# Kernel optimization log

Hardware: AMD Instinct MI355X
Metric: run time of the kernel (lower is better)

Reference implementation:

```python
import jax, jax.numpy as jnp
import numpy as np

D_IN, H, V = 512, 1024, 32000
S, B, T = 64, 128, 48
MARGIN = 0.1


def setup_inputs() -> dict:
    key = jax.random.key(0)
    ks = jax.random.split(key, 16)
    sc = 0.05
    f = lambda k, shp: jax.random.normal(k, shp, jnp.float32) * sc
    emb_W = f(ks[0], (V, D_IN)).at[0].set(0.0)  # padding_idx=0 row is zero
    return dict(
        ctx=jax.random.normal(ks[1], (S, B, H), jnp.float32),
        ctx_mask=jnp.ones((S, B), jnp.float32),
        y=jax.random.randint(ks[2], (T, B), 0, V),
        emb_W=emb_W,
        W_init=f(ks[3], (H, H)), b_init=jnp.zeros((H,), jnp.float32),
        W_ih0=f(ks[4], (3 * H, D_IN)), W_hh0=f(ks[5], (3 * H, H)),
        b_ih0=jnp.zeros((3 * H,), jnp.float32), b_hh0=jnp.zeros((3 * H,), jnp.float32),
        W_c2c=f(ks[6], (H, H)), W_h2c=f(ks[7], (H, H)), v_att=f(ks[8], (H,)),
        W_ih1=f(ks[9], (3 * H, H)), W_hh1=f(ks[10], (3 * H, H)),
        b_ih1=jnp.zeros((3 * H,), jnp.float32), b_hh1=jnp.zeros((3 * H,), jnp.float32),
        W_h2o=f(ks[11], (D_IN, H)), b_h2o=jnp.zeros((D_IN,), jnp.float32),
        W_out=f(ks[12], (V, D_IN)),
    )


def _gru(x, h, Wih, Whh, bih, bhh):
    # torch.nn.GRUCell math
    gi = x @ Wih.T + bih
    gh = h @ Whh.T + bhh
    ir, iz, inn = jnp.split(gi, 3, axis=-1)
    hr, hz, hn = jnp.split(gh, 3, axis=-1)
    r = jax.nn.sigmoid(ir + hr)
    z = jax.nn.sigmoid(iz + hz)
    n = jnp.tanh(inn + r * hn)
    return (1.0 - z) * n + z * h


def reference(ctx, ctx_mask, y, emb_W, W_init, b_init, W_ih0, W_hh0, b_ih0, b_hh0,
              W_c2c, W_h2c, v_att, W_ih1, W_hh1, b_ih1, b_hh1, W_h2o, b_h2o, W_out):
    # dec_init='mean_ctx': tanh(FF(masked mean over source))
    mean_ctx = ctx.sum(0) / ctx_mask.sum(0)[:, None]            # (B,H)
    h = jnp.tanh(mean_ctx @ W_init.T + b_init)                  # h0 (B,H)

    ctx_p = jnp.einsum('sbc,dc->sbd', ctx, W_c2c)               # ctx2ctx, hoisted out of loop
    neg = jnp.where(ctx_mask > 0, 0.0, -1e9)                    # (S,B) additive mask
    W_out_n = W_out / jnp.linalg.norm(W_out, axis=-1, keepdims=True)

    emb_in = emb_W[y[:-1]]                                      # (T-1,B,D_IN)
    targets = y[1:]                                             # (T-1,B)

    def step(h, inp):
        e, tgt = inp
        h1 = _gru(e, h, W_ih0, W_hh0, b_ih0, b_hh0)             # dec0
        # MLP attention: v^T tanh(ctx2ctx(ctx) + hid2ctx(h1))
        scores = jnp.tanh(ctx_p + (h1 @ W_h2c.T)[None]) @ v_att + neg   # (S,B)
        alpha = jax.nn.softmax(scores, axis=0)
        z_t = jnp.einsum('sb,sbc->bc', alpha, ctx)              # context (B,H)
        h2 = _gru(z_t, h1, W_ih1, W_hh1, b_ih1, b_hh1)          # dec1
        logit = jnp.tanh(h2 @ W_h2o.T + b_h2o)                  # hid2out
        logit = logit / jnp.linalg.norm(logit, axis=-1, keepdims=True)
        log_p = logit @ W_out_n.T                               # (B,V) cosine sims
        # max-margin loss, contrastive_type='max', ignore pad (tgt==0)
        s_true = jnp.take_along_axis(log_p, tgt[:, None], axis=1)
        viol = jnp.maximum(MARGIN - s_true + log_p, 0.0)
        viol = viol * (1.0 - jax.nn.one_hot(tgt, V, dtype=log_p.dtype))
        l = jnp.sum(jnp.where(tgt != 0, viol.max(-1), 0.0))
        return h2, l

    _, losses = jax.lax.scan(step, h, (emb_in, targets))
    return losses.sum()
```

## Files before the change

kernel.cpp:

```cpp
#include <hip/hip_runtime.h>
#include <math.h>

#define H    1024
#define H3   3072
#define DIN  512
#define VSZ  32000
#define SS   64
#define BB   128
#define TP   47
#define NROWS (TP*BB)
#define VCHUNKS 250
#define FMARGIN 0.1f
#define NBLK 256
#define HS   65536

typedef unsigned short u16;
typedef unsigned int u32;
typedef __bf16 bf16_t;
typedef bf16_t bf16x8 __attribute__((ext_vector_type(8)));
typedef float f32x4 __attribute__((ext_vector_type(4)));
typedef u16 u16x4 __attribute__((ext_vector_type(4)));
typedef u16 u16x8 __attribute__((ext_vector_type(8)));

#define MFMA __builtin_amdgcn_mfma_f32_16x16x32_bf16

__device__ inline u16 f2bf(float f){
    unsigned b = __float_as_uint(f);
    return (u16)((b + 0x7FFFu + ((b >> 16) & 1u)) >> 16);
}
__device__ inline float bf2f(u16 u){ return __uint_as_float(((unsigned)u) << 16); }
__device__ inline float sigm(float x){ return 1.f/(1.f + expf(-x)); }

__device__ inline void stoval(float* p, float v){ *p = v; }
__device__ inline void stoval(u16* p, float v){ *p = f2bf(v); }

__device__ inline void cstore(u32* p, u32 v){ __hip_atomic_store(p, v, __ATOMIC_RELAXED, __HIP_MEMORY_SCOPE_AGENT); }
__device__ inline void cstoref(float* p, float v){ __hip_atomic_store(p, v, __ATOMIC_RELAXED, __HIP_MEMORY_SCOPE_AGENT); }
__device__ inline float cloadf(const float* p){ return __hip_atomic_load(p, __ATOMIC_RELAXED, __HIP_MEMORY_SCOPE_AGENT); }

__device__ inline void gbar(u32* bar, u32* mygen, int tid){
    __syncthreads();
    if (tid == 0){
        u32 tgt = ++(*mygen);
        __builtin_amdgcn_s_waitcnt(0);
        u32 old = __hip_atomic_fetch_add(&bar[0], 1u, __ATOMIC_RELAXED, __HIP_MEMORY_SCOPE_AGENT);
        if (old == NBLK - 1u){
            __hip_atomic_store(&bar[0], 0u, __ATOMIC_RELAXED, __HIP_MEMORY_SCOPE_AGENT);
            __hip_atomic_store(&bar[1], tgt, __ATOMIC_RELAXED, __HIP_MEMORY_SCOPE_AGENT);
        } else {
            while (__hip_atomic_load(&bar[1], __ATOMIC_RELAXED, __HIP_MEMORY_SCOPE_AGENT) < tgt)
                __builtin_amdgcn_s_sleep(2);
        }
    }
    __syncthreads();
    asm volatile("" ::: "memory");
}


__global__ __launch_bounds__(128) void k_mask_sum(const float* __restrict__ mask, float* __restrict__ msum){
    int b = threadIdx.x;
    if (b < BB){ float s = 0.f; for (int i = 0; i < SS; i++) s += mask[i*BB + b]; msum[b] = s; }
}

__global__ __launch_bounds__(256) void k_mean_ctx(const float* __restrict__ ctx, const float* __restrict__ msum,
                                                  float* __restrict__ mean){
    int idx = blockIdx.x*256 + threadIdx.x;
    if (idx < BB*H){
        float s = 0.f;
        for (int i = 0; i < SS; i++) s += ctx[(size_t)i*BB*H + idx];
        mean[idx] = s / msum[idx / H];
    }
}

__global__ __launch_bounds__(256) void k_f32bf(const float* __restrict__ in, u16* __restrict__ out, int n4){
    int i = blockIdx.x*256 + threadIdx.x;
    if (i >= n4) return;
    float4 v = ((const float4*)in)[i];
    u16x4 o = { f2bf(v.x), f2bf(v.y), f2bf(v.z), f2bf(v.w) };
    ((u16x4*)out)[i] = o;
}

__global__ __launch_bounds__(256) void k_pack_h0(const float* __restrict__ h0, u32* __restrict__ hsHI,
                                                 u32* __restrict__ hsLO, float* __restrict__ hsF){
    int i = blockIdx.x*256 + threadIdx.x;
    float v0 = h0[i*2], v1 = h0[i*2 + 1];
    u16 a = f2bf(v0), b = f2bf(v1);
    hsHI[i] = (u32)a | ((u32)b << 16);
    hsLO[i] = (u32)f2bf(v0 - bf2f(a)) | ((u32)f2bf(v1 - bf2f(b)) << 16);
    hsF[i*2] = v0; hsF[i*2 + 1] = v1;
}

__global__ __launch_bounds__(256) void k_f2bf_frag(const float* __restrict__ in, u16* __restrict__ out,
                                                   int RK8, int K8){
    int t = blockIdx.x*256 + threadIdx.x;
    if (t >= RK8) return;
    int r = t / K8, k8 = t - r*K8;
    const float* p = in + (size_t)r*K8*8 + k8*8;
    float4 a = *(const float4*)p;
    float4 b = *(const float4*)(p + 4);
    size_t dst = ((size_t)(r >> 4)*(K8 >> 2) + (k8 >> 2))*512 + (size_t)((r & 15) + (k8 & 3)*16)*8;
    u16x8 o;
    o[0]=f2bf(a.x); o[1]=f2bf(a.y); o[2]=f2bf(a.z); o[3]=f2bf(a.w);
    o[4]=f2bf(b.x); o[5]=f2bf(b.y); o[6]=f2bf(b.z); o[7]=f2bf(b.w);
    *(u16x8*)(out + dst) = o;
}

__global__ __launch_bounds__(256) void k_rownorm_frag(const float* __restrict__ in, u16* __restrict__ out,
                                                      int nrows){
    int w = threadIdx.x >> 6, lane = threadIdx.x & 63;
    int row = blockIdx.x*4 + w;
    if (row >= nrows) return;
    const float* r = in + (size_t)row*512 + lane*8;
    float4 a = *(const float4*)r;
    float4 b = *(const float4*)(r + 4);
    float s = a.x*a.x + a.y*a.y + a.z*a.z + a.w*a.w
            + b.x*b.x + b.y*b.y + b.z*b.z + b.w*b.w;
    #pragma unroll
    for (int off = 32; off; off >>= 1) s += __shfl_xor(s, off);
    float inv = rsqrtf(s);
    size_t dst = ((size_t)(row >> 4)*16 + (lane >> 2))*512 + (size_t)((row & 15) + (lane & 3)*16)*8;
    u16x8 o;
    o[0]=f2bf(a.x*inv); o[1]=f2bf(a.y*inv); o[2]=f2bf(a.z*inv); o[3]=f2bf(a.w*inv);
    o[4]=f2bf(b.x*inv); o[5]=f2bf(b.y*inv); o[6]=f2bf(b.z*inv); o[7]=f2bf(b.w*inv);
    *(u16x8*)(out + dst) = o;
}

__global__ __launch_bounds__(256) void k_emb_frag(const float* __restrict__ emb, const int* __restrict__ y,
                                                  u16* __restrict__ out){
    int w = threadIdx.x >> 6, lane = threadIdx.x & 63;
    int row = blockIdx.x*4 + w;
    int src = y[row];
    const float* r = emb + (size_t)src*512 + lane*8;
    float4 a = *(const float4*)r;
    float4 b = *(const float4*)(r + 4);
    size_t dst = ((size_t)(row >> 4)*16 + (lane >> 2))*512 + (size_t)((row & 15) + (lane & 3)*16)*8;
    u16x8 o;
    o[0]=f2bf(a.x); o[1]=f2bf(a.y); o[2]=f2bf(a.z); o[3]=f2bf(a.w);
    o[4]=f2bf(b.x); o[5]=f2bf(b.y); o[6]=f2bf(b.z); o[7]=f2bf(b.w);
    *(u16x8*)(out + dst) = o;
}

template<int ACT>
__global__ __launch_bounds__(256) void k_gemm_nt(const float* __restrict__ A, const float* __restrict__ W,
                                                 const float* __restrict__ bias, float* __restrict__ C,
                                                 int M, int N, int K){
    __shared__ float As[16][68];
    __shared__ float Ws[16][68];
    int tid = threadIdx.x;
    int bm = blockIdx.y*64, bn = blockIdx.x*64;
    int lr = tid >> 2;
    int lk = (tid & 3) * 4;
    int tr = (tid >> 4) * 4;
    int tc = (tid & 15) * 4;
    float acc[4][4] = {};
    const float* Abase = A + (size_t)(bm + lr)*K;
    const float* Wbase = W + (size_t)(bn + lr)*K;
    for (int k0 = 0; k0 < K; k0 += 16){
        float4 av = *(const float4*)(Abase + k0 + lk);
        float4 wv = *(const float4*)(Wbase + k0 + lk);
        __syncthreads();
        As[lk+0][lr]=av.x; As[lk+1][lr]=av.y; As[lk+2][lr]=av.z; As[lk+3][lr]=av.w;
        Ws[lk+0][lr]=wv.x; Ws[lk+1][lr]=wv.y; Ws[lk+2][lr]=wv.z; Ws[lk+3][lr]=wv.w;
        __syncthreads();
        #pragma unroll
        for (int kk = 0; kk < 16; kk++){
            float4 a = *(const float4*)&As[kk][tr];
            float4 w = *(const float4*)&Ws[kk][tc];
            acc[0][0] += a.x*w.x; acc[0][1] += a.x*w.y; acc[0][2] += a.x*w.z; acc[0][3] += a.x*w.w;
            acc[1][0] += a.y*w.x; acc[1][1] += a.y*w.y; acc[1][2] += a.y*w.z; acc[1][3] += a.y*w.w;
            acc[2][0] += a.z*w.x; acc[2][1] += a.z*w.y; acc[2][2] += a.z*w.z; acc[2][3] += a.z*w.w;
            acc[3][0] += a.w*w.x; acc[3][1] += a.w*w.y; acc[3][2] += a.w*w.z; acc[3][3] += a.w*w.w;
        }
    }
    #pragma unroll
    for (int i = 0; i < 4; i++){
        #pragma unroll
        for (int j = 0; j < 4; j++){
            float v = acc[i][j];
            if (bias) v += bias[bn + tc + j];
            if (ACT == 1) v = tanhf(v);
            C[(size_t)(bm + tr + i)*N + bn + tc + j] = v;
        }
    }
}

template<int AFRAG, int ACT, typename OutT>
__global__ __launch_bounds__(256) void k_gemmf(const u16* __restrict__ A, const u16* __restrict__ B,
                                               const float* __restrict__ bias, OutT* __restrict__ C,
                                               int M, int N, int K){
    int tid = threadIdx.x, lane = tid & 63, w = tid >> 6;
    int wm = w >> 1, wn = w & 1;
    int row0 = blockIdx.y*128 + wm*64, col0 = blockIdx.x*128 + wn*64;
    int r16 = lane & 15, kg8 = (lane >> 4)*8, rg = (lane >> 4)*4;
    int K32 = K >> 5;
    f32x4 acc[4][4] = {};
    for (int k0 = 0; k0 < K32; k0++){
        bf16x8 af[4], bfv[4];
        #pragma unroll
        for (int i = 0; i < 4; i++){
            if (AFRAG) af[i] = *(const bf16x8*)(A + (((size_t)((row0 >> 4) + i)*K32 + k0) << 9) + lane*8);
            else       af[i] = *(const bf16x8*)(A + (size_t)(row0 + i*16 + r16)*K + k0*32 + kg8);
        }
        #pragma unroll
        for (int j = 0; j < 4; j++)
            bfv[j] = *(const bf16x8*)(B + (((size_t)((col0 >> 4) + j)*K32 + k0) << 9) + lane*8);
        #pragma unroll
        for (int i = 0; i < 4; i++)
            #pragma unroll
            for (int j = 0; j < 4; j++)
                acc[i][j] = MFMA(af[i], bfv[j], acc[i][j], 0, 0, 0);
    }
    #pragma unroll
    for (int i = 0; i < 4; i++){
        #pragma unroll
        for (int j = 0; j < 4; j++){
            #pragma unroll
            for (int r = 0; r < 4; r++){
                int row = row0 + i*16 + rg + r;
                int col = col0 + j*16 + r16;
                float v = acc[i][j][r];
                if (bias) v += bias[col];
                if (ACT) v = tanhf(v);
                stoval(C + (size_t)row*N + col, v);
            }
        }
    }
}

struct RD {
    const u16 *gi0, *Whh0, *Wh2c, *Wih1, *Whh1, *ctxp;
    const float *bhh0, *bih1, *bhh1, *vatt, *mask, *ctxf;
    u32 *hsHI, *hsLO, *h1HI, *h1LO, *ztHI, *ztLO;
    float *hsF, *h1F, *prF, *ghF;
    u16 *h2all;
    u32 *bar;
};

__global__ __launch_bounds__(512) void k_recur3(RD a){
    __shared__ u16 wlds[65536];
    __shared__ float ps[H];
    __shared__ float vattL[H];
    __shared__ float sal[SS];
    __shared__ float zred[4][512];
    const int tid = threadIdx.x, lane = tid & 63, wv = tid >> 6;
    const int bid = blockIdx.x;
    const int r16 = lane & 15, rg = (lane >> 4)*4, kq4 = (lane >> 4)*4;
    const int ab = (bid & 7)*16 + ((bid >> 3) >> 1);
    const int ahalf = (bid >> 3) & 1;
    u32 mygen = 0;

    {
        auto cp32k = [&](const u16* gsrc, int tile, int base){
            const u32* s = (const u32*)(gsrc + (size_t)tile*16384);
            u32* d = (u32*)(wlds + base);
            #pragma unroll
            for (int i = 0; i < 16; i++) d[tid + i*512] = s[tid + i*512];
        };
        if (bid < 64){
            cp32k(a.Whh0, bid, 0); cp32k(a.Whh0, 64+bid, 16384); cp32k(a.Whh0, 128+bid, 32768);
            cp32k(a.Whh1, bid, 49152);
        } else if (bid < 128){
            int jt = bid - 64;
            cp32k(a.Wih1, jt, 0); cp32k(a.Wih1, 64+jt, 16384); cp32k(a.Wih1, 128+jt, 32768);
            cp32k(a.Whh1, bid, 49152);
        } else if (bid < 192){
            cp32k(a.Whh1, bid, 0);
        } else {
            cp32k(a.Wh2c, bid-192, 0);
        }
        for (int i = tid; i < H; i += 512) vattL[i] = a.vatt[i];
    }
    __syncthreads();
    const int whh1_base = (bid < 128) ? 49152 : 0;

    for (int t = 0; t < TP; t++){
        if (bid < 64){
            const u32* AbH = a.hsHI + (size_t)t*HS + (size_t)(wv*16 + r16)*512 + kq4;
            const u32* AbL = a.hsLO + (size_t)t*HS + (size_t)(wv*16 + r16)*512 + kq4;
            f32x4 ac0 = {}, ac1 = {}, ac2 = {};
            for (int k0 = 0; k0 < 32; k0++){
                bf16x8 ah = *(const bf16x8*)(AbH + k0*16);
                bf16x8 al = *(const bf16x8*)(AbL + k0*16);
                bf16x8 b0 = *(const bf16x8*)(wlds + (k0*64 + lane)*8);
                bf16x8 b1 = *(const bf16x8*)(wlds + 16384 + (k0*64 + lane)*8);
                bf16x8 b2 = *(const bf16x8*)(wlds + 32768 + (k0*64 + lane)*8);
                ac0 = MFMA(ah, b0, ac0, 0, 0, 0); ac0 = MFMA(al, b0, ac0, 0, 0, 0);
                ac1 = MFMA(ah, b1, ac1, 0, 0, 0); ac1 = MFMA(al, b1, ac1, 0, 0, 0);
                ac2 = MFMA(ah, b2, ac2, 0, 0, 0); ac2 = MFMA(al, b2, ac2, 0, 0, 0);
            }
            const u16* gi = a.gi0 + (size_t)t*BB*H3;
            #pragma unroll
            for (int r = 0; r < 4; r++){
                int b = wv*16 + rg + r, j = bid*16 + r16;
                float gr = bf2f(gi[(size_t)b*H3 + j]);
                float gz = bf2f(gi[(size_t)b*H3 + H + j]);
                float gn = bf2f(gi[(size_t)b*H3 + 2*H + j]);
                float hr = ac0[r] + a.bhh0[j];
                float hz = ac1[r] + a.bhh0[H + j];
                float hn = ac2[r] + a.bhh0[2*H + j];
                float hp = cloadf(a.hsF + (size_t)b*H + j);
                float rr = sigm(gr + hr), zz = sigm(gz + hz);
                float nn = tanhf(gn + rr*hn);
                float hv = (1.f - zz)*nn + zz*hp;
                cstoref(a.h1F + (size_t)b*H + j, hv);
                u16 hib = f2bf(hv);
                u16 lob = f2bf(hv - bf2f(hib));
                u32 hip = (u32)__shfl_xor((int)(u32)hib, 1);
                u32 lop = (u32)__shfl_xor((int)(u32)lob, 1);
                if (!(r16 & 1)){
                    cstore(a.h1HI + (size_t)t*HS + (size_t)b*512 + (j >> 1), (u32)hib | (hip << 16));
                    cstore(a.h1LO + (size_t)t*HS + (size_t)b*512 + (j >> 1), (u32)lob | (lop << 16));
                }
            }
        }
        gbar(a.bar, &mygen, tid);

        {
            const u32* AbH = a.h1HI + (size_t)t*HS + (size_t)(wv*16 + r16)*512 + kq4;
            const u32* AbL = a.h1LO + (size_t)t*HS + (size_t)(wv*16 + r16)*512 + kq4;
            const u16* Bb = wlds + (bid < 192 ? whh1_base : 0);
            f32x4 ac = {};
            for (int k0 = 0; k0 < 32; k0++){
                bf16x8 ah = *(const bf16x8*)(AbH + k0*16);
                bf16x8 al = *(const bf16x8*)(AbL + k0*16);
                bf16x8 bv = *(const bf16x8*)(Bb + (k0*64 + lane)*8);
                ac = MFMA(ah, bv, ac, 0, 0, 0); ac = MFMA(al, bv, ac, 0, 0, 0);
            }
            #pragma unroll
            for (int r = 0; r < 4; r++){
                int b = wv*16 + rg + r;
                if (bid < 192) cstoref(a.ghF + (size_t)b*H3 + bid*16 + r16, ac[r]);
                else           cstoref(a.prF + (size_t)b*H + (bid - 192)*16 + r16, ac[r]);
            }
        }
        gbar(a.bar, &mygen, tid);

        {
            int b = ab;
            for (int i = tid; i < H; i += 512) ps[i] = cloadf(a.prF + (size_t)b*H + i);
            __syncthreads();
            #pragma unroll
            for (int q = 0; q < 8; q++){
                int s = wv*8 + q;
                const u16* cp = a.ctxp + ((size_t)(s*BB + b))*H + lane*16;
                u16x8 c0 = *(const u16x8*)cp;
                u16x8 c1 = *(const u16x8*)(cp + 8);
                const float* pp = ps + lane*16;
                const float* vv = vattL + lane*16;
                float acc = 0.f;
                #pragma unroll
                for (int e = 0; e < 8; e++) acc += tanhf(bf2f(c0[e]) + pp[e]) * vv[e];
                #pragma unroll
                for (int e = 0; e < 8; e++) acc += tanhf(bf2f(c1[e]) + pp[8 + e]) * vv[8 + e];
                #pragma unroll
                for (int off = 32; off; off >>= 1) acc += __shfl_xor(acc, off);
                if (lane == 0) sal[s] = acc + ((a.mask[s*BB + b] > 0.f) ? 0.f : -1e9f);
            }
            __syncthreads();
            if (tid < 64){
                float v = sal[tid];
                float m = v;
                #pragma unroll
                for (int off = 32; off; off >>= 1) m = fmaxf(m, __shfl_xor(m, off));
                float e = expf(v - m);
                float su = e;
                #pragma unroll
                for (int off = 32; off; off >>= 1) su += __shfl_xor(su, off);
                sal[tid] = e / su;
            }
            __syncthreads();
            int cq = (tid & 127)*4, sg = tid >> 7;
            float4 z = {0.f, 0.f, 0.f, 0.f};
            for (int si = 0; si < 16; si++){
                int s = sg + si*4;
                float al = sal[s];
                float4 cv = *(const float4*)(a.ctxf + ((size_t)(s*BB + b))*H + ahalf*512 + cq);
                z.x += al*cv.x; z.y += al*cv.y; z.z += al*cv.z; z.w += al*cv.w;
            }
            *(float4*)&zred[sg][cq] = z;
            __syncthreads();
            if (tid < 256){
                int c2 = tid*2;
                float a0 = zred[0][c2]   + zred[1][c2]   + zred[2][c2]   + zred[3][c2];
                float a1 = zred[0][c2+1] + zred[1][c2+1] + zred[2][c2+1] + zred[3][c2+1];
                int j0 = ahalf*512 + c2;
                u16 h0b = f2bf(a0), h1b = f2bf(a1);
                cstore(a.ztHI + (size_t)t*HS + (size_t)b*512 + (j0 >> 1), (u32)h0b | ((u32)h1b << 16));
                cstore(a.ztLO + (size_t)t*HS + (size_t)b*512 + (j0 >> 1),
                       (u32)f2bf(a0 - bf2f(h0b)) | ((u32)f2bf(a1 - bf2f(h1b)) << 16));
            }
            __syncthreads();
        }
        gbar(a.bar, &mygen, tid);

        if (bid >= 64 && bid < 128){
            int jt = bid - 64;
            const u32* AbH = a.ztHI + (size_t)t*HS + (size_t)(wv*16 + r16)*512 + kq4;
            const u32* AbL = a.ztLO + (size_t)t*HS + (size_t)(wv*16 + r16)*512 + kq4;
            f32x4 ac0 = {}, ac1 = {}, ac2 = {};
            for (int k0 = 0; k0 < 32; k0++){
                bf16x8 ah = *(const bf16x8*)(AbH + k0*16);
                bf16x8 al = *(const bf16x8*)(AbL + k0*16);
                bf16x8 b0 = *(const bf16x8*)(wlds + (k0*64 + lane)*8);
                bf16x8 b1 = *(const bf16x8*)(wlds + 16384 + (k0*64 + lane)*8);
                bf16x8 b2 = *(const bf16x8*)(wlds + 32768 + (k0*64 + lane)*8);
                ac0 = MFMA(ah, b0, ac0, 0, 0, 0); ac0 = MFMA(al, b0, ac0, 0, 0, 0);
                ac1 = MFMA(ah, b1, ac1, 0, 0, 0); ac1 = MFMA(al, b1, ac1, 0, 0, 0);
                ac2 = MFMA(ah, b2, ac2, 0, 0, 0); ac2 = MFMA(al, b2, ac2, 0, 0, 0);
            }
            #pragma unroll
            for (int r = 0; r < 4; r++){
                int b = wv*16 + rg + r, j = jt*16 + r16;
                float gr = ac0[r] + a.bih1[j];
                float gz = ac1[r] + a.bih1[H + j];
                float gn = ac2[r] + a.bih1[2*H + j];
                float hr = cloadf(a.ghF + (size_t)b*H3 + j)       + a.bhh1[j];
                float hz = cloadf(a.ghF + (size_t)b*H3 + H + j)   + a.bhh1[H + j];
                float hn = cloadf(a.ghF + (size_t)b*H3 + 2*H + j) + a.bhh1[2*H + j];
                float h1v = cloadf(a.h1F + (size_t)b*H + j);
                float rr = sigm(gr + hr), zz = sigm(gz + hz);
                float nn = tanhf(gn + rr*hn);
                float hv = (1.f - zz)*nn + zz*h1v;
                cstoref(a.hsF + (size_t)b*H + j, hv);
                a.h2all[((size_t)t*BB + b)*H + j] = f2bf(hv);
                u16 hib = f2bf(hv);
                u16 lob = f2bf(hv - bf2f(hib));
                u32 hip = (u32)__shfl_xor((int)(u32)hib, 1);
                u32 lop = (u32)__shfl_xor((int)(u32)lob, 1);
                if (!(r16 & 1)){
                    cstore(a.hsHI + (size_t)(t+1)*HS + (size_t)b*512 + (j >> 1), (u32)hib | (hip << 16));
                    cstore(a.hsLO + (size_t)(t+1)*HS + (size_t)b*512 + (j >> 1), (u32)lob | (lop << 16));
                }
            }
        }
        gbar(a.bar, &mygen, tid);
    }
}

__global__ __launch_bounds__(256) void k_final(const u16* __restrict__ logitf, const u16* __restrict__ Wf,
                                               const int* __restrict__ y, float* __restrict__ pmax,
                                               float* __restrict__ strue){
    __shared__ float red[128][2];
    int tid = threadIdx.x, w = tid >> 6, lane = tid & 63;
    int wm = w >> 1, wn = w & 1;
    int row0 = blockIdx.x*128 + wm*64;
    int col0 = blockIdx.y*128 + wn*64;
    int r16 = lane & 15, rg = (lane >> 4)*4;
    f32x4 acc[4][4] = {};
    for (int k0 = 0; k0 < 16; k0++){
        bf16x8 af[4], bfv[4];
        #pragma unroll
        for (int i = 0; i < 4; i++)
            af[i] = *(const bf16x8*)(logitf + (((size_t)((row0 >> 4) + i)*16 + k0) << 9) + lane*8);
        #pragma unroll
        for (int j = 0; j < 4; j++)
            bfv[j] = *(const bf16x8*)(Wf + (((size_t)((col0 >> 4) + j)*16 + k0) << 9) + lane*8);
        #pragma unroll
        for (int i = 0; i < 4; i++)
            #pragma unroll
            for (int j = 0; j < 4; j++)
                acc[i][j] = MFMA(af[i], bfv[j], acc[i][j], 0, 0, 0);
    }
    #pragma unroll
    for (int i = 0; i < 4; i++){
        #pragma unroll
        for (int r = 0; r < 4; r++){
            int row = row0 + i*16 + rg + r;
            int tgt = y[row + BB];
            float m = -1e30f;
            #pragma unroll
            for (int j = 0; j < 4; j++){
                float v = acc[i][j][r];
                int col = col0 + j*16 + r16;
                if (col == tgt){ strue[row] = v; v = -1e30f; }
                m = fmaxf(m, v);
            }
            m = fmaxf(m, __shfl_xor(m, 1));
            m = fmaxf(m, __shfl_xor(m, 2));
            m = fmaxf(m, __shfl_xor(m, 4));
            m = fmaxf(m, __shfl_xor(m, 8));
            if (r16 == 0) red[wm*64 + i*16 + rg + r][wn] = m;
        }
    }
    __syncthreads();
    if (tid < 128){
        float m = fmaxf(red[tid][0], red[tid][1]);
        pmax[(size_t)(blockIdx.x*128 + tid)*VCHUNKS + blockIdx.y] = m;
    }
}

__global__ __launch_bounds__(256) void k_loss(const float* __restrict__ pmax, const float* __restrict__ strue,
                                              const int* __restrict__ y, float* __restrict__ out){
    int R = blockIdx.x*256 + threadIdx.x;
    int lane = threadIdx.x & 63, wave = threadIdx.x >> 6;
    float l = 0.f;
    if (R < NROWS){
        int tgt = y[R + BB];
        if (tgt != 0){
            const float* pm = pmax + (size_t)R*VCHUNKS;
            float m = -1e30f;
            for (int i = 0; i < VCHUNKS; i++) m = fmaxf(m, pm[i]);
            l = fmaxf(FMARGIN - strue[R] + m, 0.f);
        }
    }
    #pragma unroll
    for (int off = 32; off; off >>= 1) l += __shfl_down(l, off);
    __shared__ float wsum[4];
    if (lane == 0) wsum[wave] = l;
    __syncthreads();
    if (threadIdx.x == 0) atomicAdd(out, wsum[0] + wsum[1] + wsum[2] + wsum[3]);
}

extern "C" void kernel_launch(void* const* d_in, const int* in_sizes, int n_in,
                              void* d_out, int out_size, void* d_ws, size_t ws_size,
                              hipStream_t stream){
    const float* ctx    = (const float*)d_in[0];
    const float* mask   = (const float*)d_in[1];
    const int*   y      = (const int*)d_in[2];
    const float* emb_W  = (const float*)d_in[3];
    const float* W_init = (const float*)d_in[4];
    const float* b_init = (const float*)d_in[5];
    const float* W_ih0  = (const float*)d_in[6];
    const float* W_hh0  = (const float*)d_in[7];
    const float* b_ih0  = (const float*)d_in[8];
    const float* b_hh0  = (const float*)d_in[9];
    const float* W_c2c  = (const float*)d_in[10];
    const float* W_h2c  = (const float*)d_in[11];
    const float* v_att  = (const float*)d_in[12];
    const float* W_ih1  = (const float*)d_in[13];
    const float* W_hh1  = (const float*)d_in[14];
    const float* b_ih1  = (const float*)d_in[15];
    const float* b_hh1  = (const float*)d_in[16];
    const float* W_h2o  = (const float*)d_in[17];
    const float* b_h2o  = (const float*)d_in[18];
    const float* W_out  = (const float*)d_in[19];
    float* out = (float*)d_out;

    char* wsb = (char*)d_ws;
    size_t off = 0;
    auto alloc = [&](size_t bytes)->void*{
        void* p = (void*)(wsb + off);
        off = (off + bytes + 255) & ~(size_t)255;
        return p;
    };
    u16* Wih0f = (u16*)alloc((size_t)H3*DIN*2);
    u16* Whh0f = (u16*)alloc((size_t)H3*H*2);
    u16* Wih1f = (u16*)alloc((size_t)H3*H*2);
    u16* Whh1f = (u16*)alloc((size_t)H3*H*2);
    u16* Wh2cf = (u16*)alloc((size_t)H*H*2);
    u16* Wc2cf = (u16*)alloc((size_t)H*H*2);
    u16* Wh2of = (u16*)alloc((size_t)DIN*H*2);
    u16* Woutf = (u16*)alloc((size_t)VSZ*DIN*2);
    u16* ctxb  = (u16*)alloc((size_t)SS*BB*H*2);
    u16* ctxpb = (u16*)alloc((size_t)SS*BB*H*2);
    u16* embf  = (u16*)alloc((size_t)NROWS*DIN*2);
    u16* gi0b  = (u16*)alloc((size_t)NROWS*H3*2);
    u16* h2allb= (u16*)alloc((size_t)NROWS*H*2);
    u32* hsHI  = (u32*)alloc((size_t)(TP+1)*HS*4);
    u32* hsLO  = (u32*)alloc((size_t)(TP+1)*HS*4);
    u32* h1HI  = (u32*)alloc((size_t)TP*HS*4);
    u32* h1LO  = (u32*)alloc((size_t)TP*HS*4);
    u32* ztHI  = (u32*)alloc((size_t)TP*HS*4);
    u32* ztLO  = (u32*)alloc((size_t)TP*HS*4);
    float* hsF = (float*)alloc((size_t)BB*H*4);
    float* h1F = (float*)alloc((size_t)BB*H*4);
    float* prF = (float*)alloc((size_t)BB*H*4);
    float* ghF = (float*)alloc((size_t)BB*H3*4);
    u32* bar   = (u32*)alloc(256);
    float* strue  = (float*)alloc(NROWS*4);
    float* msum   = (float*)alloc(BB*4);
    float* meanc  = (float*)alloc((size_t)BB*H*4);
    float* h0f    = (float*)alloc((size_t)BB*H*4);

    float* logitf  = (float*)gi0b;
    u16*   logitfr = (u16*)(gi0b + (size_t)NROWS*DIN*2);
    float* pmax    = (float*)(gi0b + (size_t)NROWS*DIN*2 + (size_t)NROWS*DIN);

    hipMemsetAsync(d_out, 0, sizeof(float), stream);
    hipMemsetAsync(bar, 0, 256, stream);

    hipLaunchKernelGGL(k_mask_sum, dim3(1), dim3(128), 0, stream, mask, msum);
    hipLaunchKernelGGL(k_mean_ctx, dim3(BB*H/256), dim3(256), 0, stream, ctx, msum, meanc);
    hipLaunchKernelGGL((k_gemm_nt<1>), dim3(H/64, BB/64), dim3(256), 0, stream,
                       meanc, W_init, b_init, h0f, BB, H, H);
    hipLaunchKernelGGL(k_pack_h0, dim3(HS/256), dim3(256), 0, stream, h0f, hsHI, hsLO, hsF);

    hipLaunchKernelGGL(k_f2bf_frag, dim3(H3*DIN/8/256), dim3(256), 0, stream, W_ih0, Wih0f, H3*DIN/8, DIN/8);
    hipLaunchKernelGGL(k_f2bf_frag, dim3(H3*H/8/256), dim3(256), 0, stream, W_hh0, Whh0f, H3*H/8, H/8);
    hipLaunchKernelGGL(k_f2bf_frag, dim3(H3*H/8/256), dim3(256), 0, stream, W_ih1, Wih1f, H3*H/8, H/8);
    hipLaunchKernelGGL(k_f2bf_frag, dim3(H3*H/8/256), dim3(256), 0, stream, W_hh1, Whh1f, H3*H/8, H/8);
    hipLaunchKernelGGL(k_f2bf_frag, dim3(H*H/8/256), dim3(256), 0, stream, W_h2c, Wh2cf, H*H/8, H/8);
    hipLaunchKernelGGL(k_f2bf_frag, dim3(H*H/8/256), dim3(256), 0, stream, W_c2c, Wc2cf, H*H/8, H/8);
    hipLaunchKernelGGL(k_f2bf_frag, dim3(DIN*H/8/256), dim3(256), 0, stream, W_h2o, Wh2of, DIN*H/8, H/8);
    hipLaunchKernelGGL(k_rownorm_frag, dim3(VSZ/4), dim3(256), 0, stream, W_out, Woutf, VSZ);
    hipLaunchKernelGGL(k_f32bf, dim3(SS*BB*H/4/256), dim3(256), 0, stream, ctx, ctxb, SS*BB*H/4);
    hipLaunchKernelGGL(k_emb_frag, dim3(NROWS/4), dim3(256), 0, stream, emb_W, y, embf);

    hipLaunchKernelGGL((k_gemmf<1,0,u16>), dim3(H3/128, NROWS/128), dim3(256), 0, stream,
                       embf, Wih0f, b_ih0, gi0b, NROWS, H3, DIN);
    hipLaunchKernelGGL((k_gemmf<0,0,u16>), dim3(H/128, SS*BB/128), dim3(256), 0, stream,
                       ctxb, Wc2cf, (const float*)nullptr, ctxpb, SS*BB, H, H);

    RD rd;
    rd.gi0 = gi0b; rd.Whh0 = Whh0f; rd.Wh2c = Wh2cf; rd.Wih1 = Wih1f; rd.Whh1 = Whh1f;
    rd.ctxp = ctxpb;
    rd.bhh0 = b_hh0; rd.bih1 = b_ih1; rd.bhh1 = b_hh1; rd.vatt = v_att; rd.mask = mask; rd.ctxf = ctx;
    rd.hsHI = hsHI; rd.hsLO = hsLO; rd.h1HI = h1HI; rd.h1LO = h1LO; rd.ztHI = ztHI; rd.ztLO = ztLO;
    rd.hsF = hsF; rd.h1F = h1F; rd.prF = prF; rd.ghF = ghF;
    rd.h2all = h2allb; rd.bar = bar;
    void* kp[] = { (void*)&rd };
    hipLaunchCooperativeKernel((const void*)k_recur3, dim3(NBLK), dim3(512), kp, 0, stream);

    hipLaunchKernelGGL((k_gemmf<0,1,float>), dim3(DIN/128, NROWS/128), dim3(256), 0, stream,
                       h2allb, Wh2of, b_h2o, logitf, NROWS, DIN, H);
    hipLaunchKernelGGL(k_rownorm_frag, dim3(NROWS/4), dim3(256), 0, stream, logitf, logitfr, NROWS);
    hipLaunchKernelGGL(k_final, dim3(NROWS/128, VSZ/128), dim3(256), 0, stream,
                       logitfr, Woutf, y, pmax, strue);
    hipLaunchKernelGGL(k_loss, dim3((NROWS + 255)/256), dim3(256), 0, stream, pmax, strue, y, out);
}
```

Baseline: 5.726 ms.

## Spread GRU gate GEMMs across 192 blocks and split out elementwise gate phase

The recurrent cooperative kernel previously computed the dec0 and dec1 GRU gate GEMMs on only 64 blocks each, with three accumulators per block and the gate nonlinearity fused in. Now 192 blocks each compute one 16-column gate tile into new global buffers g0/g1. A separate elementwise phase over all 256 blocks then applies the GRU update, which costs two extra grid barriers per timestep and an extra global round trip. It also pads the shared attention vectors (ps, vattL) with a stride-17 layout to avoid LDS bank conflicts, and shrinks the shared weight buffer.

After: 5.809 ms. About the same (+1.4%).

```diff
diff --git a/kernel.cpp b/kernel.cpp
--- a/kernel.cpp
+++ b/kernel.cpp
@@ -13,6 +13,7 @@
 #define FMARGIN 0.1f
 #define NBLK 256
 #define HS   65536
+#define PS(i) ((i) + ((i) >> 4))
 
 typedef unsigned short u16;
 typedef unsigned int u32;
@@ -227,19 +228,19 @@
     }
 }
 
-struct RD {
+struct RE {
     const u16 *gi0, *Whh0, *Wh2c, *Wih1, *Whh1, *ctxp;
     const float *bhh0, *bih1, *bhh1, *vatt, *mask, *ctxf;
     u32 *hsHI, *hsLO, *h1HI, *h1LO, *ztHI, *ztLO;
-    float *hsF, *h1F, *prF, *ghF;
+    float *hsF, *h1F, *prF, *ghF, *g0, *g1;
     u16 *h2all;
     u32 *bar;
 };
 
-__global__ __launch_bounds__(512) void k_recur3(RD a){
-    __shared__ u16 wlds[65536];
-    __shared__ float ps[H];
-    __shared__ float vattL[H];
+__global__ __launch_bounds__(512) void k_recur4(RE a){
+    __shared__ u16 wlds[49152];
+    __shared__ float ps[1088];
+    __shared__ float vattL[1088];
     __shared__ float sal[SS];
     __shared__ float zred[4][512];
     const int tid = threadIdx.x, lane = tid & 63, wv = tid >> 6;
@@ -256,69 +257,63 @@
             #pragma unroll
             for (int i = 0; i < 16; i++) d[tid + i*512] = s[tid + i*512];
         };
-        if (bid < 64){
-            cp32k(a.Whh0, bid, 0); cp32k(a.Whh0, 64+bid, 16384); cp32k(a.Whh0, 128+bid, 32768);
-            cp32k(a.Whh1, bid, 49152);
-        } else if (bid < 128){
-            int jt = bid - 64;
-            cp32k(a.Wih1, jt, 0); cp32k(a.Wih1, 64+jt, 16384); cp32k(a.Wih1, 128+jt, 32768);
-            cp32k(a.Whh1, bid, 49152);
-        } else if (bid < 192){
-            cp32k(a.Whh1, bid, 0);
+        if (bid < 192){
+            cp32k(a.Whh0, bid, 0);
+            cp32k(a.Wih1, bid, 16384);
+            cp32k(a.Whh1, bid, 32768);
         } else {
             cp32k(a.Wh2c, bid-192, 0);
         }
-        for (int i = tid; i < H; i += 512) vattL[i] = a.vatt[i];
+        for (int i = tid; i < H; i += 512) vattL[PS(i)] = a.vatt[i];
     }
     __syncthreads();
-    const int whh1_base = (bid < 128) ? 49152 : 0;
 
     for (int t = 0; t < TP; t++){
-        if (bid < 64){
+        if (bid < 192){
             const u32* AbH = a.hsHI + (size_t)t*HS + (size_t)(wv*16 + r16)*512 + kq4;
             const u32* AbL = a.hsLO + (size_t)t*HS + (size_t)(wv*16 + r16)*512 + kq4;
-            f32x4 ac0 = {}, ac1 = {}, ac2 = {};
+            f32x4 ac = {};
             for (int k0 = 0; k0 < 32; k0++){
                 bf16x8 ah = *(const bf16x8*)(AbH + k0*16);
                 bf16x8 al = *(const bf16x8*)(AbL + k0*16);
-                bf16x8 b0 = *(const bf16x8*)(wlds + (k0*64 + lane)*8);
-                bf16x8 b1 = *(const bf16x8*)(wlds + 16384 + (k0*64 + lane)*8);
-                bf16x8 b2 = *(const bf16x8*)(wlds + 32768 + (k0*64 + lane)*8);
-                ac0 = MFMA(ah, b0, ac0, 0, 0, 0); ac0 = MFMA(al, b0, ac0, 0, 0, 0);
-                ac1 = MFMA(ah, b1, ac1, 0, 0, 0); ac1 = MFMA(al, b1, ac1, 0, 0, 0);
-                ac2 = MFMA(ah, b2, ac2, 0, 0, 0); ac2 = MFMA(al, b2, ac2, 0, 0, 0);
-            }
-            const u16* gi = a.gi0 + (size_t)t*BB*H3;
-            #pragma unroll
-            for (int r = 0; r < 4; r++){
-                int b = wv*16 + rg + r, j = bid*16 + r16;
-                float gr = bf2f(gi[(size_t)b*H3 + j]);
-                float gz = bf2f(gi[(size_t)b*H3 + H + j]);
-                float gn = bf2f(gi[(size_t)b*H3 + 2*H + j]);
-                float hr = ac0[r] + a.bhh0[j];
-                float hz = ac1[r] + a.bhh0[H + j];
-                float hn = ac2[r] + a.bhh0[2*H + j];
-                float hp = cloadf(a.hsF + (size_t)b*H + j);
-                float rr = sigm(gr + hr), zz = sigm(gz + hz);
-                float nn = tanhf(gn + rr*hn);
-                float hv = (1.f - zz)*nn + zz*hp;
-                cstoref(a.h1F + (size_t)b*H + j, hv);
-                u16 hib = f2bf(hv);
-                u16 lob = f2bf(hv - bf2f(hib));
-                u32 hip = (u32)__shfl_xor((int)(u32)hib, 1);
-                u32 lop = (u32)__shfl_xor((int)(u32)lob, 1);
-                if (!(r16 & 1)){
-                    cstore(a.h1HI + (size_t)t*HS + (size_t)b*512 + (j >> 1), (u32)hib | (hip << 16));
-                    cstore(a.h1LO + (size_t)t*HS + (size_t)b*512 + (j >> 1), (u32)lob | (lop << 16));
-                }
-            }
+                bf16x8 bw = *(const bf16x8*)(wlds + (k0*64 + lane)*8);
+                ac = MFMA(ah, bw, ac, 0, 0, 0); ac = MFMA(al, bw, ac, 0, 0, 0);
+            }
+            #pragma unroll
+            for (int r = 0; r < 4; r++)
+                cstoref(a.g0 + (size_t)(wv*16 + rg + r)*H3 + bid*16 + r16, ac[r]);
+        }
+        gbar(a.bar, &mygen, tid);
+
+        if (tid < 256){
+            int q = bid*256 + tid;
+            int b = q >> 9, jp = q & 511, j = jp*2;
+            const u16* gi = a.gi0 + (size_t)t*BB*H3 + (size_t)b*H3;
+            float hv[2];
+            #pragma unroll
+            for (int e = 0; e < 2; e++){
+                int jj = j + e;
+                float gr = bf2f(gi[jj])       + cloadf(a.g0 + (size_t)b*H3 + jj)       + a.bhh0[jj];
+                float gz = bf2f(gi[H + jj])   + cloadf(a.g0 + (size_t)b*H3 + H + jj)   + a.bhh0[H + jj];
+                float gni = bf2f(gi[2*H + jj]);
+                float gnh = cloadf(a.g0 + (size_t)b*H3 + 2*H + jj) + a.bhh0[2*H + jj];
+                float rr = sigm(gr), zz = sigm(gz);
+                float nn = tanhf(gni + rr*gnh);
+                float hp = cloadf(a.hsF + (size_t)b*H + jj);
+                hv[e] = (1.f - zz)*nn + zz*hp;
+                cstoref(a.h1F + (size_t)b*H + jj, hv[e]);
+            }
+            u16 i0 = f2bf(hv[0]), i1 = f2bf(hv[1]);
+            cstore(a.h1HI + (size_t)t*HS + (size_t)b*512 + jp, (u32)i0 | ((u32)i1 << 16));
+            cstore(a.h1LO + (size_t)t*HS + (size_t)b*512 + jp,
+                   (u32)f2bf(hv[0] - bf2f(i0)) | ((u32)f2bf(hv[1] - bf2f(i1)) << 16));
         }
         gbar(a.bar, &mygen, tid);
 
         {
             const u32* AbH = a.h1HI + (size_t)t*HS + (size_t)(wv*16 + r16)*512 + kq4;
             const u32* AbL = a.h1LO + (size_t)t*HS + (size_t)(wv*16 + r16)*512 + kq4;
-            const u16* Bb = wlds + (bid < 192 ? whh1_base : 0);
+            const u16* Bb = wlds + (bid < 192 ? 32768 : 0);
             f32x4 ac = {};
             for (int k0 = 0; k0 < 32; k0++){
                 bf16x8 ah = *(const bf16x8*)(AbH + k0*16);
@@ -337,7 +332,7 @@
 
         {
             int b = ab;
-            for (int i = tid; i < H; i += 512) ps[i] = cloadf(a.prF + (size_t)b*H + i);
+            for (int i = tid; i < H; i += 512) ps[PS(i)] = cloadf(a.prF + (size_t)b*H + i);
             __syncthreads();
             #pragma unroll
             for (int q = 0; q < 8; q++){
@@ -345,8 +340,8 @@
                 const u16* cp = a.ctxp + ((size_t)(s*BB + b))*H + lane*16;
                 u16x8 c0 = *(const u16x8*)cp;
                 u16x8 c1 = *(const u16x8*)(cp + 8);
-                const float* pp = ps + lane*16;
-                const float* vv = vattL + lane*16;
+                const float* pp = ps + lane*17;
+                const float* vv = vattL + lane*17;
                 float acc = 0.f;
                 #pragma unroll
                 for (int e = 0; e < 8; e++) acc += tanhf(bf2f(c0[e]) + pp[e]) * vv[e];
@@ -384,54 +379,55 @@
                 float a0 = zred[0][c2]   + zred[1][c2]   + zred[2][c2]   + zred[3][c2];
                 float a1 = zred[0][c2+1] + zred[1][c2+1] + zred[2][c2+1] + zred[3][c2+1];
                 int j0 = ahalf*512 + c2;
-                u16 h0b = f2bf(a0), h1b = f2bf(a1);
-                cstore(a.ztHI + (size_t)t*HS + (size_t)b*512 + (j0 >> 1), (u32)h0b | ((u32)h1b << 16));
+                u16 z0 = f2bf(a0), z1 = f2bf(a1);
+                cstore(a.ztHI + (size_t)t*HS + (size_t)b*512 + (j0 >> 1), (u32)z0 | ((u32)z1 << 16));
                 cstore(a.ztLO + (size_t)t*HS + (size_t)b*512 + (j0 >> 1),
-                       (u32)f2bf(a0 - bf2f(h0b)) | ((u32)f2bf(a1 - bf2f(h1b)) << 16));
+                       (u32)f2bf(a0 - bf2f(z0)) | ((u32)f2bf(a1 - bf2f(z1)) << 16));
             }
             __syncthreads();
         }
         gbar(a.bar, &mygen, tid);
 
-        if (bid >= 64 && bid < 128){
-            int jt = bid - 64;
+        if (bid < 192){
             const u32* AbH = a.ztHI + (size_t)t*HS + (size_t)(wv*16 + r16)*512 + kq4;
             const u32* AbL = a.ztLO + (size_t)t*HS + (size_t)(wv*16 + r16)*512 + kq4;
-            f32x4 ac0 = {}, ac1 = {}, ac2 = {};
+            f32x4 ac = {};
             for (int k0 = 0; k0 < 32; k0++){
                 bf16x8 ah = *(const bf16x8*)(AbH + k0*16);
                 bf16x8 al = *(const bf16x8*)(AbL + k0*16);
-                bf16x8 b0 = *(const bf16x8*)(wlds + (k0*64 + lane)*8);
-                bf16x8 b1 = *(const bf16x8*)(wlds + 16384 + (k0*64 + lane)*8);
-                bf16x8 b2 = *(const bf16x8*)(wlds + 32768 + (k0*64 + lane)*8);
-                ac0 = MFMA(ah, b0, ac0, 0, 0, 0); ac0 = MFMA(al, b0, ac0, 0, 0, 0);
-                ac1 = MFMA(ah, b1, ac1, 0, 0, 0); ac1 = MFMA(al, b1, ac1, 0, 0, 0);
-                ac2 = MFMA(ah, b2, ac2, 0, 0, 0); ac2 = MFMA(al, b2, ac2, 0, 0, 0);
-            }
-            #pragma unroll
-            for (int r = 0; r < 4; r++){
-                int b = wv*16 + rg + r, j = jt*16 + r16;
-                float gr = ac0[r] + a.bih1[j];
-                float gz = ac1[r] + a.bih1[H + j];
-                float gn = ac2[r] + a.bih1[2*H + j];
-                float hr = cloadf(a.ghF + (size_t)b*H3 + j)       + a.bhh1[j];
-                float hz = cloadf(a.ghF + (size_t)b*H3 + H + j)   + a.bhh1[H + j];
-                float hn = cloadf(a.ghF + (size_t)b*H3 + 2*H + j) + a.bhh1[2*H + j];
-                float h1v = cloadf(a.h1F + (size_t)b*H + j);
+                bf16x8 bw = *(const bf16x8*)(wlds + 16384 + (k0*64 + lane)*8);
+                ac = MFMA(ah, bw, ac, 0, 0, 0); ac = MFMA(al, bw, ac, 0, 0, 0);
+            }
+            #pragma unroll
+            for (int r = 0; r < 4; r++)
+                cstoref(a.g1 + (size_t)(wv*16 + rg + r)*H3 + bid*16 + r16, ac[r]);
+        }
+        gbar(a.bar, &mygen, tid);
+
+        if (tid < 256){
+            int q = bid*256 + tid;
+            int b = q >> 9, jp = q & 511, j = jp*2;
+            float hv[2];
+            #pragma unroll
+            for (int e = 0; e < 2; e++){
+                int jj = j + e;
+                float gr = cloadf(a.g1 + (size_t)b*H3 + jj)       + a.bih1[jj];
+                float gz = cloadf(a.g1 + (size_t)b*H3 + H + jj)   + a.bih1[H + jj];
+                float gn = cloadf(a.g1 + (size_t)b*H3 + 2*H + jj) + a.bih1[2*H + jj];
+                float hr = cloadf(a.ghF + (size_t)b*H3 + jj)       + a.bhh1[jj];
+                float hz = cloadf(a.ghF + (size_t)b*H3 + H + jj)   + a.bhh1[H + jj];
+                float hn = cloadf(a.ghF + (size_t)b*H3 + 2*H + jj) + a.bhh1[2*H + jj];
                 float rr = sigm(gr + hr), zz = sigm(gz + hz);
                 float nn = tanhf(gn + rr*hn);
-                float hv = (1.f - zz)*nn + zz*h1v;
-                cstoref(a.hsF + (size_t)b*H + j, hv);
-                a.h2all[((size_t)t*BB + b)*H + j] = f2bf(hv);
-                u16 hib = f2bf(hv);
-                u16 lob = f2bf(hv - bf2f(hib));
-                u32 hip = (u32)__shfl_xor((int)(u32)hib, 1);
-                u32 lop = (u32)__shfl_xor((int)(u32)lob, 1);
-                if (!(r16 & 1)){
-                    cstore(a.hsHI + (size_t)(t+1)*HS + (size_t)b*512 + (j >> 1), (u32)hib | (hip << 16));
-                    cstore(a.hsLO + (size_t)(t+1)*HS + (size_t)b*512 + (j >> 1), (u32)lob | (lop << 16));
-                }
-            }
+                float h1v = cloadf(a.h1F + (size_t)b*H + jj);
+                hv[e] = (1.f - zz)*nn + zz*h1v;
+                cstoref(a.hsF + (size_t)b*H + jj, hv[e]);
+                a.h2all[((size_t)t*BB + b)*H + jj] = f2bf(hv[e]);
+            }
+            u16 i0 = f2bf(hv[0]), i1 = f2bf(hv[1]);
+            cstore(a.hsHI + (size_t)(t+1)*HS + (size_t)b*512 + jp, (u32)i0 | ((u32)i1 << 16));
+            cstore(a.hsLO + (size_t)(t+1)*HS + (size_t)b*512 + jp,
+                   (u32)f2bf(hv[0] - bf2f(i0)) | ((u32)f2bf(hv[1] - bf2f(i1)) << 16));
         }
         gbar(a.bar, &mygen, tid);
     }
@@ -566,6 +562,8 @@
     float* h1F = (float*)alloc((size_t)BB*H*4);
     float* prF = (float*)alloc((size_t)BB*H*4);
     float* ghF = (float*)alloc((size_t)BB*H3*4);
+    float* g0  = (float*)alloc((size_t)BB*H3*4);
+    float* g1  = (float*)alloc((size_t)BB*H3*4);
     u32* bar   = (u32*)alloc(256);
     float* strue  = (float*)alloc(NROWS*4);
     float* msum   = (float*)alloc(BB*4);
@@ -601,15 +599,15 @@
     hipLaunchKernelGGL((k_gemmf<0,0,u16>), dim3(H/128, SS*BB/128), dim3(256), 0, stream,
                        ctxb, Wc2cf, (const float*)nullptr, ctxpb, SS*BB, H, H);
 
-    RD rd;
-    rd.gi0 = gi0b; rd.Whh0 = Whh0f; rd.Wh2c = Wh2cf; rd.Wih1 = Wih1f; rd.Whh1 = Whh1f;
-    rd.ctxp = ctxpb;
-    rd.bhh0 = b_hh0; rd.bih1 = b_ih1; rd.bhh1 = b_hh1; rd.vatt = v_att; rd.mask = mask; rd.ctxf = ctx;
-    rd.hsHI = hsHI; rd.hsLO = hsLO; rd.h1HI = h1HI; rd.h1LO = h1LO; rd.ztHI = ztHI; rd.ztLO = ztLO;
-    rd.hsF = hsF; rd.h1F = h1F; rd.prF = prF; rd.ghF = ghF;
-    rd.h2all = h2allb; rd.bar = bar;
-    void* kp[] = { (void*)&rd };
-    hipLaunchCooperativeKernel((const void*)k_recur3, dim3(NBLK), dim3(512), kp, 0, stream);
+    RE re;
+    re.gi0 = gi0b; re.Whh0 = Whh0f; re.Wh2c = Wh2cf; re.Wih1 = Wih1f; re.Whh1 = Whh1f;
+    re.ctxp = ctxpb;
+    re.bhh0 = b_hh0; re.bih1 = b_ih1; re.bhh1 = b_hh1; re.vatt = v_att; re.mask = mask; re.ctxf = ctx;
+    re.hsHI = hsHI; re.hsLO = hsLO; re.h1HI = h1HI; re.h1LO = h1LO; re.ztHI = ztHI; re.ztLO = ztLO;
+    re.hsF = hsF; re.h1F = h1F; re.prF = prF; re.ghF = ghF; re.g0 = g0; re.g1 = g1;
+    re.h2all = h2allb; re.bar = bar;
+    void* kp[] = { (void*)&re };
+    hipLaunchCooperativeKernel((const void*)k_recur4, dim3(NBLK), dim3(512), kp, 0, stream);
 
     hipLaunchKernelGGL((k_gemmf<0,1,float>), dim3(DIN/128, NROWS/128), dim3(256), 0, stream,
                        h2allb, Wh2of, b_h2o, logitf, NROWS, DIN, H);
```

## Use hierarchical grid barrier and rebalance Whh1 work onto fewer blocks

Applied to the files above, without the earlier changes.

Replaces the flat single-counter grid barrier with a two-level one: blocks first arrive on one of 32 per-group counters (8 blocks each, padded apart), and the last arriver per group bumps a top-level counter. This is meant to cut atomic contention on a single address at every phase. The Whh1 gate GEMM moves from 192 blocks with one 16-column tile each to blocks 128-191 with three tiles each. That shrinks per-block LDS and lets the other blocks skip that phase, but it lengthens the critical path on those blocks. Shared arrays for the attention projection and v_att also get padded indexing to avoid LDS bank conflicts.

New measurement: 5.929 ms. +3.6%, slower.

```diff
diff --git a/kernel.cpp b/kernel.cpp
--- a/kernel.cpp
+++ b/kernel.cpp
@@ -13,6 +13,7 @@
 #define FMARGIN 0.1f
 #define NBLK 256
 #define HS   65536
+#define PS(i) ((i) + ((i) >> 4))
 
 typedef unsigned short u16;
 typedef unsigned int u32;
@@ -38,19 +39,23 @@
 __device__ inline void cstoref(float* p, float v){ __hip_atomic_store(p, v, __ATOMIC_RELAXED, __HIP_MEMORY_SCOPE_AGENT); }
 __device__ inline float cloadf(const float* p){ return __hip_atomic_load(p, __ATOMIC_RELAXED, __HIP_MEMORY_SCOPE_AGENT); }
 
-__device__ inline void gbar(u32* bar, u32* mygen, int tid){
+__device__ inline void gbar(u32* bar, u32* mygen, int tid, int bid){
     __syncthreads();
     if (tid == 0){
         u32 tgt = ++(*mygen);
         __builtin_amdgcn_s_waitcnt(0);
-        u32 old = __hip_atomic_fetch_add(&bar[0], 1u, __ATOMIC_RELAXED, __HIP_MEMORY_SCOPE_AGENT);
-        if (old == NBLK - 1u){
-            __hip_atomic_store(&bar[0], 0u, __ATOMIC_RELAXED, __HIP_MEMORY_SCOPE_AGENT);
-            __hip_atomic_store(&bar[1], tgt, __ATOMIC_RELAXED, __HIP_MEMORY_SCOPE_AGENT);
-        } else {
-            while (__hip_atomic_load(&bar[1], __ATOMIC_RELAXED, __HIP_MEMORY_SCOPE_AGENT) < tgt)
-                __builtin_amdgcn_s_sleep(2);
-        }
+        u32* cnt = bar + 64 + (bid >> 3)*32;
+        u32 old = __hip_atomic_fetch_add(cnt, 1u, __ATOMIC_RELAXED, __HIP_MEMORY_SCOPE_AGENT);
+        if (old == 7u){
+            __hip_atomic_store(cnt, 0u, __ATOMIC_RELAXED, __HIP_MEMORY_SCOPE_AGENT);
+            u32 old2 = __hip_atomic_fetch_add(&bar[1], 1u, __ATOMIC_RELEASE, __HIP_MEMORY_SCOPE_AGENT);
+            if (old2 == 31u){
+                __hip_atomic_store(&bar[1], 0u, __ATOMIC_RELAXED, __HIP_MEMORY_SCOPE_AGENT);
+                __hip_atomic_store(&bar[0], tgt, __ATOMIC_RELEASE, __HIP_MEMORY_SCOPE_AGENT);
+            }
+        }
+        while (__hip_atomic_load(&bar[0], __ATOMIC_RELAXED, __HIP_MEMORY_SCOPE_AGENT) < tgt)
+            __builtin_amdgcn_s_sleep(1);
     }
     __syncthreads();
     asm volatile("" ::: "memory");
@@ -227,7 +232,7 @@
     }
 }
 
-struct RD {
+struct RF {
     const u16 *gi0, *Whh0, *Wh2c, *Wih1, *Whh1, *ctxp;
     const float *bhh0, *bih1, *bhh1, *vatt, *mask, *ctxf;
     u32 *hsHI, *hsLO, *h1HI, *h1LO, *ztHI, *ztLO;
@@ -236,10 +241,10 @@
     u32 *bar;
 };
 
-__global__ __launch_bounds__(512) void k_recur3(RD a){
-    __shared__ u16 wlds[65536];
-    __shared__ float ps[H];
-    __shared__ float vattL[H];
+__global__ __launch_bounds__(512) void k_recur5(RF a){
+    __shared__ u16 wlds[49152];
+    __shared__ float ps[1088];
+    __shared__ float vattL[1088];
     __shared__ float sal[SS];
     __shared__ float zred[4][512];
     const int tid = threadIdx.x, lane = tid & 63, wv = tid >> 6;
@@ -258,20 +263,18 @@
         };
         if (bid < 64){
             cp32k(a.Whh0, bid, 0); cp32k(a.Whh0, 64+bid, 16384); cp32k(a.Whh0, 128+bid, 32768);
-            cp32k(a.Whh1, bid, 49152);
         } else if (bid < 128){
             int jt = bid - 64;
             cp32k(a.Wih1, jt, 0); cp32k(a.Wih1, 64+jt, 16384); cp32k(a.Wih1, 128+jt, 32768);
-            cp32k(a.Whh1, bid, 49152);
         } else if (bid < 192){
-            cp32k(a.Whh1, bid, 0);
+            int wt = bid - 128;
+            cp32k(a.Whh1, 3*wt, 0); cp32k(a.Whh1, 3*wt+1, 16384); cp32k(a.Whh1, 3*wt+2, 32768);
         } else {
             cp32k(a.Wh2c, bid-192, 0);
         }
-        for (int i = tid; i < H; i += 512) vattL[i] = a.vatt[i];
+        for (int i = tid; i < H; i += 512) vattL[PS(i)] = a.vatt[i];
     }
     __syncthreads();
-    const int whh1_base = (bid < 128) ? 49152 : 0;
 
     for (int t = 0; t < TP; t++){
         if (bid < 64){
@@ -313,31 +316,52 @@
                 }
             }
         }
-        gbar(a.bar, &mygen, tid);
-
-        {
+        gbar(a.bar, &mygen, tid, bid);
+
+        if (bid >= 128){
             const u32* AbH = a.h1HI + (size_t)t*HS + (size_t)(wv*16 + r16)*512 + kq4;
             const u32* AbL = a.h1LO + (size_t)t*HS + (size_t)(wv*16 + r16)*512 + kq4;
-            const u16* Bb = wlds + (bid < 192 ? whh1_base : 0);
-            f32x4 ac = {};
-            for (int k0 = 0; k0 < 32; k0++){
-                bf16x8 ah = *(const bf16x8*)(AbH + k0*16);
-                bf16x8 al = *(const bf16x8*)(AbL + k0*16);
-                bf16x8 bv = *(const bf16x8*)(Bb + (k0*64 + lane)*8);
-                ac = MFMA(ah, bv, ac, 0, 0, 0); ac = MFMA(al, bv, ac, 0, 0, 0);
-            }
-            #pragma unroll
-            for (int r = 0; r < 4; r++){
-                int b = wv*16 + rg + r;
-                if (bid < 192) cstoref(a.ghF + (size_t)b*H3 + bid*16 + r16, ac[r]);
-                else           cstoref(a.prF + (size_t)b*H + (bid - 192)*16 + r16, ac[r]);
-            }
-        }
-        gbar(a.bar, &mygen, tid);
+            if (bid < 192){
+                int wt = bid - 128;
+                f32x4 ac0 = {}, ac1 = {}, ac2 = {};
+                for (int k0 = 0; k0 < 32; k0++){
+                    bf16x8 ah = *(const bf16x8*)(AbH + k0*16);
+                    bf16x8 al = *(const bf16x8*)(AbL + k0*16);
+                    bf16x8 b0 = *(const bf16x8*)(wlds + (k0*64 + lane)*8);
+                    bf16x8 b1 = *(const bf16x8*)(wlds + 16384 + (k0*64 + lane)*8);
+                    bf16x8 b2 = *(const bf16x8*)(wlds + 32768 + (k0*64 + lane)*8);
+                    ac0 = MFMA(ah, b0, ac0, 0, 0, 0); ac0 = MFMA(al, b0, ac0, 0, 0, 0);
+                    ac1 = MFMA(ah, b1, ac1, 0, 0, 0); ac1 = MFMA(al, b1, ac1, 0, 0, 0);
+                    ac2 = MFMA(ah, b2, ac2, 0, 0, 0); ac2 = MFMA(al, b2, ac2, 0, 0, 0);
+                }
+                #pragma unroll
+                for (int r = 0; r < 4; r++){
+                    int b = wv*16 + rg + r;
+                    int c0 = wt*48 + r16;
+                    cstoref(a.ghF + (size_t)b*H3 + c0,      ac0[r]);
+                    cstoref(a.ghF + (size_t)b*H3 + c0 + 16, ac1[r]);
+                    cstoref(a.ghF + (size_t)b*H3 + c0 + 32, ac2[r]);
+                }
+            } else {
+                f32x4 ac = {};
+                for (int k0 = 0; k0 < 32; k0++){
+                    bf16x8 ah = *(const bf16x8*)(AbH + k0*16);
+                    bf16x8 al = *(const bf16x8*)(AbL + k0*16);
+                    bf16x8 bv = *(const bf16x8*)(wlds + (k0*64 + lane)*8);
+                    ac = MFMA(ah, bv, ac, 0, 0, 0); ac = MFMA(al, bv, ac, 0, 0, 0);
+                }
+                #pragma unroll
+                for (int r = 0; r < 4; r++){
+                    int b = wv*16 + rg + r;
+                    cstoref(a.prF + (size_t)b*H + (bid - 192)*16 + r16, ac[r]);
+                }
+            }
+        }
+        gbar(a.bar, &mygen, tid, bid);
 
         {
             int b = ab;
-            for (int i = tid; i < H; i += 512) ps[i] = cloadf(a.prF + (size_t)b*H + i);
+            for (int i = tid; i < H; i += 512) ps[PS(i)] = cloadf(a.prF + (size_t)b*H + i);
             __syncthreads();
             #pragma unroll
             for (int q = 0; q < 8; q++){
@@ -345,8 +369,8 @@
                 const u16* cp = a.ctxp + ((size_t)(s*BB + b))*H + lane*16;
                 u16x8 c0 = *(const u16x8*)cp;
                 u16x8 c1 = *(const u16x8*)(cp + 8);
-                const float* pp = ps + lane*16;
-                const float* vv = vattL + lane*16;
+                const float* pp = ps + lane*17;
+                const float* vv = vattL + lane*17;
                 float acc = 0.f;
                 #pragma unroll
                 for (int e = 0; e < 8; e++) acc += tanhf(bf2f(c0[e]) + pp[e]) * vv[e];
@@ -384,14 +408,14 @@
                 float a0 = zred[0][c2]   + zred[1][c2]   + zred[2][c2]   + zred[3][c2];
                 float a1 = zred[0][c2+1] + zred[1][c2+1] + zred[2][c2+1] + zred[3][c2+1];
                 int j0 = ahalf*512 + c2;
-                u16 h0b = f2bf(a0), h1b = f2bf(a1);
-                cstore(a.ztHI + (size_t)t*HS + (size_t)b*512 + (j0 >> 1), (u32)h0b | ((u32)h1b << 16));
+                u16 z0 = f2bf(a0), z1 = f2bf(a1);
+                cstore(a.ztHI + (size_t)t*HS + (size_t)b*512 + (j0 >> 1), (u32)z0 | ((u32)z1 << 16));
                 cstore(a.ztLO + (size_t)t*HS + (size_t)b*512 + (j0 >> 1),
-                       (u32)f2bf(a0 - bf2f(h0b)) | ((u32)f2bf(a1 - bf2f(h1b)) << 16));
+                       (u32)f2bf(a0 - bf2f(z0)) | ((u32)f2bf(a1 - bf2f(z1)) << 16));
             }
             __syncthreads();
         }
-        gbar(a.bar, &mygen, tid);
+        gbar(a.bar, &mygen, tid, bid);
 
         if (bid >= 64 && bid < 128){
             int jt = bid - 64;
@@ -433,7 +457,7 @@
                 }
             }
         }
-        gbar(a.bar, &mygen, tid);
+        gbar(a.bar, &mygen, tid, bid);
     }
 }
 
@@ -566,7 +590,7 @@
     float* h1F = (float*)alloc((size_t)BB*H*4);
     float* prF = (float*)alloc((size_t)BB*H*4);
     float* ghF = (float*)alloc((size_t)BB*H3*4);
-    u32* bar   = (u32*)alloc(256);
+    u32* bar   = (u32*)alloc(8192);
     float* strue  = (float*)alloc(NROWS*4);
     float* msum   = (float*)alloc(BB*4);
     float* meanc  = (float*)alloc((size_t)BB*H*4);
@@ -577,7 +601,7 @@
     float* pmax    = (float*)(gi0b + (size_t)NROWS*DIN*2 + (size_t)NROWS*DIN);
 
     hipMemsetAsync(d_out, 0, sizeof(float), stream);
-    hipMemsetAsync(bar, 0, 256, stream);
+    hipMemsetAsync(bar, 0, 8192, stream);
 
     hipLaunchKernelGGL(k_mask_sum, dim3(1), dim3(128), 0, stream, mask, msum);
     hipLaunchKernelGGL(k_mean_ctx, dim3(BB*H/256), dim3(256), 0, stream, ctx, msum, meanc);
@@ -601,15 +625,15 @@
     hipLaunchKernelGGL((k_gemmf<0,0,u16>), dim3(H/128, SS*BB/128), dim3(256), 0, stream,
                        ctxb, Wc2cf, (const float*)nullptr, ctxpb, SS*BB, H, H);
 
-    RD rd;
-    rd.gi0 = gi0b; rd.Whh0 = Whh0f; rd.Wh2c = Wh2cf; rd.Wih1 = Wih1f; rd.Whh1 = Whh1f;
-    rd.ctxp = ctxpb;
-    rd.bhh0 = b_hh0; rd.bih1 = b_ih1; rd.bhh1 = b_hh1; rd.vatt = v_att; rd.mask = mask; rd.ctxf = ctx;
-    rd.hsHI = hsHI; rd.hsLO = hsLO; rd.h1HI = h1HI; rd.h1LO = h1LO; rd.ztHI = ztHI; rd.ztLO = ztLO;
-    rd.hsF = hsF; rd.h1F = h1F; rd.prF = prF; rd.ghF = ghF;
-    rd.h2all = h2allb; rd.bar = bar;
-    void* kp[] = { (void*)&rd };
-    hipLaunchCooperativeKernel((const void*)k_recur3, dim3(NBLK), dim3(512), kp, 0, stream);
+    RF rf;
+    rf.gi0 = gi0b; rf.Whh0 = Whh0f; rf.Wh2c = Wh2cf; rf.Wih1 = Wih1f; rf.Whh1 = Whh1f;
+    rf.ctxp = ctxpb;
+    rf.bhh0 = b_hh0; rf.bih1 = b_ih1; rf.bhh1 = b_hh1; rf.vatt = v_att; rf.mask = mask; rf.ctxf = ctx;
+    rf.hsHI = hsHI; rf.hsLO = hsLO; rf.h1HI = h1HI; rf.h1LO = h1LO; rf.ztHI = ztHI; rf.ztLO = ztLO;
+    rf.hsF = hsF; rf.h1F = h1F; rf.prF = prF; rf.ghF = ghF;
+    rf.h2all = h2allb; rf.bar = bar;
+    void* kp[] = { (void*)&rf };
+    hipLaunchCooperativeKernel((const void*)k_recur5, dim3(NBLK), dim3(512), kp, 0, stream);
 
     hipLaunchKernelGGL((k_gemmf<0,1,float>), dim3(DIN/128, NROWS/128), dim3(256), 0, stream,
                        h2allb, Wh2of, b_h2o, logitf, NROWS, DIN, H);
```
